# Performance work log

Hardware: AMD Instinct MI355X
Metric: run time of the kernel (lower is better)

Reference implementation:

```python
import jax, jax.numpy as jnp
import numpy as np

POOL_SIZE = 8
SEG_LEN = 100
N_CODEBOOKS = 4
VOCAB = 1024
EMB = 128
HID = 512
LAT = 256
NUM_CODES = 1024
BETA = 0.1
BATCH = 128


def _pool_matrix(T, P):
    # torch adaptive_avg_pool1d bin boundaries
    starts = np.floor(np.arange(P) * T / P).astype(int)
    ends = np.ceil((np.arange(P) + 1) * T / P).astype(int)
    M = np.zeros((T, P), np.float32)
    for i in range(P):
        M[starts[i]:ends[i], i] = 1.0 / (ends[i] - starts[i])
    return jnp.asarray(M)

_POOL = _pool_matrix(SEG_LEN, POOL_SIZE)


def _conv1d_same3(x, w, b):
    # x: (B, Cin, T), w: (Cout, Cin, 3), padding=1
    y = jax.lax.conv_general_dilated(x, w, (1,), [(1, 1)],
                                     dimension_numbers=('NCH', 'OIH', 'NCH'))
    return y + b[None, :, None]


def _encode(tokens, emb, c1w, c1b, c2w, c2b, c3w, c3b):
    # tokens: (B, T, C) int -> z_e (B, POOL_SIZE, LAT)
    B, T, C = tokens.shape
    x = emb[tokens]                      # (B, T, C, EMB)
    x = x.reshape(B, T, C * EMB).transpose(0, 2, 1)  # (B, C*EMB, T)
    x = jax.nn.relu(_conv1d_same3(x, c1w, c1b))
    x = jax.nn.relu(_conv1d_same3(x, c2w, c2b))
    x = jnp.einsum('bct,tp->bcp', x, _POOL)          # adaptive avg pool -> (B, HID, 8)
    x = jnp.einsum('bcp,oc->bpo', x, c3w[:, :, 0]) + c3b  # 1x1 conv -> (B, 8, LAT)
    return x


def _vq(z_e, codebook):
    # z_e: (B, L, D); eval-mode EMA quantizer (no buffer update)
    cb_sq = jnp.sum(codebook ** 2, axis=-1)          # (K,)
    dist = (jnp.sum(z_e ** 2, axis=-1, keepdims=True)
            - 2.0 * jnp.einsum('bld,kd->blk', z_e, codebook) + cb_sq)
    codes = jnp.argmin(dist, axis=-1)                # (B, L)
    z_q = codebook[codes]                            # gather (B, L, D)
    z_q_st = z_e + jax.lax.stop_gradient(z_q - z_e)
    commit = jnp.mean((z_e - jax.lax.stop_gradient(z_q)) ** 2)
    return z_q_st, codes, BETA * commit


def _decode(z_prev, z_curr, z_next, fc1w, fc1b, fc2w, fc2b, d1w, d1b, d2w, d2b):
    B = z_curr.shape[0]
    z = jnp.concatenate([z_prev, z_curr, z_next], axis=1).reshape(B, -1)  # (B, 3*8*LAT)
    h = jax.nn.relu(z @ fc1w.T + fc1b)
    h = jax.nn.relu(h @ fc2w.T + fc2b)               # (B, HID)
    h = jnp.broadcast_to(h[:, :, None], (B, HID, SEG_LEN))
    # ConvTranspose1d(k=3, pad=1, stride=1) == conv with flipped, transposed kernel
    w1 = jnp.flip(jnp.swapaxes(d1w, 0, 1), -1)       # (O, I, 3)
    h = jax.nn.relu(_conv1d_same3(h, w1, d1b))
    out = jnp.einsum('bct,cv->bvt', h, d2w[:, :, 0]) + d2b[None, :, None]  # (B, V*C, T)
    logits = out.reshape(B, N_CODEBOOKS, VOCAB, SEG_LEN).transpose(0, 3, 1, 2)
    return logits                                    # (B, T, C, V)


def _model(tokens_prev, tokens_curr, tokens_next, emb, conv1_w, conv1_b,
           conv2_w, conv2_b, conv3_w, conv3_b, codebook, fc1_w, fc1_b,
           fc2_w, fc2_b, deconv1_w, deconv1_b, deconv2_w, deconv2_b):
    enc = lambda t: _encode(t, emb, conv1_w, conv1_b, conv2_w, conv2_b, conv3_w, conv3_b)
    z_prev, _, vq_prev = _vq(enc(tokens_prev), codebook)
    z_curr, _, vq_curr = _vq(enc(tokens_curr), codebook)
    z_next, _, vq_next = _vq(enc(tokens_next), codebook)
    logits = _decode(z_prev, z_curr, z_next, fc1_w, fc1_b, fc2_w, fc2_b,
                     deconv1_w, deconv1_b, deconv2_w, deconv2_b)
    logp = jax.nn.log_softmax(logits, axis=-1)
    nll = -jnp.take_along_axis(logp, tokens_curr[..., None], axis=-1)[..., 0]
    recon_loss = jnp.mean(nll)
    vq_loss = vq_prev + vq_curr + vq_next
    centered = codebook - jnp.mean(codebook, axis=0, keepdims=True)
    diversity_loss = -jnp.mean(centered ** 2)
    total = recon_loss + vq_loss + 0.0 * diversity_loss  # variance_loss_scale=0.0
    return total


def setup_inputs() -> dict:
    key = jax.random.key(0)
    ks = jax.random.split(key, 20)
    s = 0.02
    n = lambda k, shape, sc=0.02: sc * jax.random.normal(k, shape, dtype=jnp.float32)
    return {
        'tokens_prev': jax.random.randint(ks[0], (BATCH, SEG_LEN, N_CODEBOOKS), 0, VOCAB),
        'tokens_curr': jax.random.randint(ks[1], (BATCH, SEG_LEN, N_CODEBOOKS), 0, VOCAB),
        'tokens_next': jax.random.randint(ks[2], (BATCH, SEG_LEN, N_CODEBOOKS), 0, VOCAB),
        'emb': n(ks[3], (VOCAB, EMB), 1.0),
        'conv1_w': n(ks[4], (HID, EMB * N_CODEBOOKS, 3)),
        'conv1_b': jnp.zeros((HID,), jnp.float32),
        'conv2_w': n(ks[5], (HID, HID, 3)),
        'conv2_b': jnp.zeros((HID,), jnp.float32),
        'conv3_w': n(ks[6], (LAT, HID, 1)),
        'conv3_b': jnp.zeros((LAT,), jnp.float32),
        'codebook': n(ks[7], (NUM_CODES, LAT), 1.0),
        'fc1_w': n(ks[8], (HID, LAT * POOL_SIZE * 3)),
        'fc1_b': jnp.zeros((HID,), jnp.float32),
        'fc2_w': n(ks[9], (HID, HID)),
        'fc2_b': jnp.zeros((HID,), jnp.float32),
        'deconv1_w': n(ks[10], (HID, HID, 3)),
        'deconv1_b': jnp.zeros((HID,), jnp.float32),
        'deconv2_w': n(ks[11], (HID, VOCAB * N_CODEBOOKS, 1)),
        'deconv2_b': jnp.zeros((VOCAB * N_CODEBOOKS,), jnp.float32),
    }


def reference(tokens_prev, tokens_curr, tokens_next, emb, conv1_w, conv1_b,
              conv2_w, conv2_b, conv3_w, conv3_b, codebook, fc1_w, fc1_b,
              fc2_w, fc2_b, deconv1_w, deconv1_b, deconv2_w, deconv2_b):
    return _model(tokens_prev, tokens_curr, tokens_next, emb, conv1_w, conv1_b,
                  conv2_w, conv2_b, conv3_w, conv3_b, codebook, fc1_w, fc1_b,
                  fc2_w, fc2_b, deconv1_w, deconv1_b, deconv2_w, deconv2_b)
```

## Files before the change

kernel.cpp:

```cpp
#include <hip/hip_runtime.h>
#include <math.h>

#define B_    128
#define T_    100
#define TPAD  104
#define CB_   4
#define EMB_  128
#define NROW  39936
#define ZOFF  131072

typedef __attribute__((ext_vector_type(8))) short short8;
typedef __attribute__((ext_vector_type(4))) short short4v;
typedef __attribute__((ext_vector_type(4))) float f32x4;

__device__ __forceinline__ short f2bf(float x) {
  unsigned u = __builtin_bit_cast(unsigned, x);
  u += 0x7fffu + ((u >> 16) & 1u);
  return (short)(u >> 16);
}
__device__ __forceinline__ float bf2f(short s) {
  unsigned u = ((unsigned)(unsigned short)s) << 16;
  return __builtin_bit_cast(float, u);
}

#define GLOAD_LDS(g, l) __builtin_amdgcn_global_load_lds( \
    (const __attribute__((address_space(1))) void*)(g),   \
    (__attribute__((address_space(3))) void*)(l), 16, 0, 0)

#define MFMA16(a, b, c) __builtin_amdgcn_mfma_f32_16x16x32_bf16(a, b, c, 0, 0, 0)
#define SWZ(row, slot) (((slot) + ((row) >> 1)) & 3)

__global__ void k_prep(const float* __restrict__ emb,
                       const float* __restrict__ c1w, const float* __restrict__ c2w,
                       const float* __restrict__ c3w, const float* __restrict__ cbk,
                       const float* __restrict__ fc1w, const float* __restrict__ fc2w,
                       const float* __restrict__ d1w, const float* __restrict__ d2w,
                       short* __restrict__ YbS, short* __restrict__ embB,
                       short* __restrict__ Wb1, short* __restrict__ Wb2,
                       short* __restrict__ c3wB, short* __restrict__ cbkB,
                       short* __restrict__ fc1wB, short* __restrict__ fc2wB,
                       short* __restrict__ SB, short* __restrict__ d2wTB,
                       float* __restrict__ cbsq) {
  __shared__ float tile[32][33];
  int bid = blockIdx.x;
  int id = bid * 256 + threadIdx.x;
  if (bid < 24581) {
    if (id < 1024) {
      int row = id >> 9, c = id & 511;
      long off = row ? ((long)(NROW + 1) * 512 + c) : c;
      YbS[off] = 0;
    } else if (id < 132096) {
      int l = id - 1024;
      embB[l] = f2bf(emb[l]);
    } else if (id < 132224) {
      embB[ZOFF + (id - 132096)] = 0;
    } else if (id < 1705088) {
      int local = id - 132224;
      const float* w = (local < 786432) ? c1w : c2w;
      short* o = (local < 786432) ? Wb1 : Wb2;
      int l2 = (local < 786432) ? local : local - 786432;
      int i = l2 & 511, oo = (l2 >> 9) & 511, tap = l2 >> 18;
      o[l2] = f2bf(w[oo * 1536 + i * 3 + tap]);
    } else if (id < 1836160) {
      int l = id - 1705088;
      c3wB[l] = f2bf(c3w[l]);
    } else if (id < 2098304) {
      int l = id - 1836160;
      cbkB[l] = f2bf(cbk[l]);
    } else if (id < 5244032) {
      int l = id - 2098304;
      fc1wB[l] = f2bf(fc1w[l]);
    } else if (id < 5506176) {
      int l = id - 5244032;
      fc2wB[l] = f2bf(fc2w[l]);
    } else if (id < 6292608) {
      int l = id - 5506176;
      int i = l & 511, o = (l >> 9) & 511, cls = l >> 18;
      const float* w = d1w + (i * 512 + o) * 3;
      float v;
      if (cls == 0)      v = w[0] + w[1];
      else if (cls == 1) v = w[0] + w[1] + w[2];
      else               v = w[1] + w[2];
      SB[(cls * 512 + o) * 512 + i] = f2bf(v);
    }
  } else if (bid < 26629) {
    int blk = bid - 24581;
    int bx = blk & 127, by = blk >> 7;
    int tx = threadIdx.x & 31, ty = threadIdx.x >> 5;
    #pragma unroll
    for (int j = 0; j < 32; j += 8)
      tile[ty + j][tx] = d2w[(by * 32 + ty + j) * 4096 + bx * 32 + tx];
    __syncthreads();
    #pragma unroll
    for (int j = 0; j < 32; j += 8)
      d2wTB[(bx * 32 + ty + j) * 512 + by * 32 + tx] = f2bf(tile[tx][ty + j]);
  } else {
    int idx = (bid - 26629) * 256 + threadIdx.x;
    int row = idx >> 6, lane = threadIdx.x & 63;
    float4 v = *(const float4*)&cbk[row * 256 + lane * 4];
    float s = v.x * v.x + v.y * v.y + v.z * v.z + v.w * v.w;
    #pragma unroll
    for (int m = 1; m < 64; m <<= 1) s += __shfl_xor(s, m);
    if (lane == 0) cbsq[row] = s;
  }
}

__global__ __launch_bounds__(256) void k_conv1_embed(const int* __restrict__ tok0,
                                                     const int* __restrict__ tok1,
                                                     const int* __restrict__ tok2,
                                                     const short* __restrict__ embB,
                                                     const short* __restrict__ Wb,
                                                     const float* __restrict__ bias,
                                                     short* __restrict__ Y) {
  __shared__ short sm[16896];
  int r0 = blockIdx.y * 128;
  int o0 = blockIdx.x * 128;
  int tid = threadIdx.x;
  int lane = tid & 63, wid = tid >> 6;
  int wm = wid >> 1, wn = wid & 1;
  int ls = lane >> 4, lr = lane & 15;
  int g = ((lane & 3) - ((lane >> 3) & 3)) & 3;

  int toff[3][4];
  #pragma unroll
  for (int i = 0; i < 3; ++i) {
    int q = wid + 4 * i;
    if (q < 9) {
      int rr = r0 - 1 + 16 * q + (lane >> 2);
      bool ok = (rr >= 0) && (rr < NROW);
      int sb = ok ? (rr / 104) : 0;
      int t = rr - sb * 104;
      ok = ok && (t < T_);
      int b = sb & 127, s = sb >> 7;
      const int* tokp = (s == 0) ? tok0 : (s == 1) ? tok1 : tok2;
      if (ok) {
        int4 tv = *(const int4*)&tokp[(b * T_ + t) * CB_];
        toff[i][0] = tv.x * EMB_; toff[i][1] = tv.y * EMB_;
        toff[i][2] = tv.z * EMB_; toff[i][3] = tv.w * EMB_;
      } else {
        toff[i][0] = toff[i][1] = toff[i][2] = toff[i][3] = ZOFF;
      }
    }
  }
  const short* gpw[9];
  short* lpw[9];
  #pragma unroll
  for (int i = 0; i < 9; ++i) {
    int q = wid + 4 * i;
    if (q >= 9 && q < 33) {
      int b = q - 9, tap = b >> 3, jj = b & 7;
      gpw[i] = Wb + (long)(tap * 512 + o0 + 16 * jj) * 512 + (long)(lane >> 2) * 512 + g * 8;
      lpw[i] = sm + q * 512;
    }
  }

  f32x4 acc[4][4] = {};
  #pragma unroll
  for (int cb = 0; cb < 4; ++cb) {
    #pragma unroll
    for (int kk = 0; kk < 4; ++kk) {
      __syncthreads();
      #pragma unroll
      for (int i = 0; i < 3; ++i) {
        int q = wid + 4 * i;
        if (q < 9) GLOAD_LDS(embB + toff[i][cb] + kk * 32 + g * 8, sm + q * 512);
      }
      #pragma unroll
      for (int i = 0; i < 9; ++i) {
        int q = wid + 4 * i;
        if (q >= 9 && q < 33) {
          GLOAD_LDS(gpw[i], lpw[i]);
          gpw[i] += 32;
        }
      }
      __syncthreads();
      const short8* A8 = (const short8*)sm;
      const short8* B8 = (const short8*)(sm + 4608);
      #pragma unroll
      for (int tap = 0; tap < 3; ++tap) {
        short8 a[4], b[4];
        #pragma unroll
        for (int m = 0; m < 4; ++m) {
          int row = wm * 64 + m * 16 + lr + tap;
          a[m] = A8[row * 4 + SWZ(row, ls)];
        }
        #pragma unroll
        for (int n = 0; n < 4; ++n) {
          int row = wn * 64 + n * 16 + lr;
          b[n] = B8[(tap * 128 + row) * 4 + SWZ(row, ls)];
        }
        #pragma unroll
        for (int m = 0; m < 4; ++m)
          #pragma unroll
          for (int n = 0; n < 4; ++n)
            acc[m][n] = MFMA16(a[m], b[n], acc[m][n]);
      }
    }
  }
  #pragma unroll
  for (int m = 0; m < 4; ++m) {
    #pragma unroll
    for (int n = 0; n < 4; ++n) {
      int col = o0 + wn * 64 + n * 16 + lr;
      float bv = bias[col];
      #pragma unroll
      for (int j = 0; j < 4; ++j) {
        int r = r0 + wm * 64 + m * 16 + ls * 4 + j;
        int t = r % TPAD;
        float v = (t < T_) ? fmaxf(acc[m][n][j] + bv, 0.f) : 0.f;
        Y[(long)r * 512 + col] = f2bf(v);
      }
    }
  }
}

__global__ __launch_bounds__(256) void k_conv3_mfma(const short* __restrict__ X,
                                                    const short* __restrict__ Wb,
                                                    const float* __restrict__ bias,
                                                    short* __restrict__ Y) {
  __shared__ short sm[16896];
  int r0 = blockIdx.y * 128;
  int o0 = blockIdx.x * 128;
  int tid = threadIdx.x;
  int lane = tid & 63, wid = tid >> 6;
  int wm = wid >> 1, wn = wid & 1;
  int ls = lane >> 4, lr = lane & 15;
  int g = ((lane & 3) - ((lane >> 3) & 3)) & 3;
  long laneoff = (long)(lane >> 2) * 512 + g * 8;

  const short* gp[9];
  const short* lp[9];
  #pragma unroll
  for (int i = 0; i < 9; ++i) {
    int q = wid + 4 * i;
    if (q < 33) {
      long base;
      const short* src;
      if (q < 9) { src = X; base = (long)(r0 - 1 + 16 * q) * 512; }
      else {
        int b = q - 9, tap = b >> 3, j = b & 7;
        src = Wb; base = (long)(tap * 512 + o0 + 16 * j) * 512;
      }
      gp[i] = src + base + laneoff;
      lp[i] = sm + q * 512;
    }
  }

  f32x4 acc[4][4] = {};
  for (int kc = 0; kc < 512; kc += 32) {
    __syncthreads();
    #pragma unroll
    for (int i = 0; i < 9; ++i) {
      int q = wid + 4 * i;
      if (q < 33) {
        GLOAD_LDS(gp[i], lp[i]);
        gp[i] += 32;
      }
    }
    __syncthreads();
    const short8* A8 = (const short8*)sm;
    const short8* B8 = (const short8*)(sm + 4608);
    #pragma unroll
    for (int tap = 0; tap < 3; ++tap) {
      short8 a[4], b[4];
      #pragma unroll
      for (int m = 0; m < 4; ++m) {
        int row = wm * 64 + m * 16 + lr + tap;
        a[m] = A8[row * 4 + SWZ(row, ls)];
      }
      #pragma unroll
      for (int n = 0; n < 4; ++n) {
        int row = wn * 64 + n * 16 + lr;
        b[n] = B8[(tap * 128 + row) * 4 + SWZ(row, ls)];
      }
      #pragma unroll
      for (int m = 0; m < 4; ++m)
        #pragma unroll
        for (int n = 0; n < 4; ++n)
          acc[m][n] = MFMA16(a[m], b[n], acc[m][n]);
    }
  }
  #pragma unroll
  for (int m = 0; m < 4; ++m) {
    #pragma unroll
    for (int n = 0; n < 4; ++n) {
      int col = o0 + wn * 64 + n * 16 + lr;
      float bv = bias[col];
      #pragma unroll
      for (int j = 0; j < 4; ++j) {
        int r = r0 + wm * 64 + m * 16 + ls * 4 + j;
        int t = r % TPAD;
        float v = (t < T_) ? fmaxf(acc[m][n][j] + bv, 0.f) : 0.f;
        Y[(long)r * 512 + col] = f2bf(v);
      }
    }
  }
}

__global__ __launch_bounds__(256) void k_gemm_mfma(const short* __restrict__ A,
                                                   const short* __restrict__ B,
                                                   float* __restrict__ C,
                                                   short* __restrict__ Cb,
                                                   const float* __restrict__ bias,
                                                   int K, int N, int relu) {
  __shared__ short sm[8192];
  int r0 = blockIdx.x * 128;
  int o0 = blockIdx.y * 128;
  int tid = threadIdx.x;
  int lane = tid & 63, wid = tid >> 6;
  int wm = wid >> 1, wn = wid & 1;
  int ls = lane >> 4, lr = lane & 15;
  int g = ((lane & 3) - ((lane >> 3) & 3)) & 3;
  long laneoff = (long)(lane >> 2) * K + g * 8;

  const short* gp[4];
  const short* lp[4];
  #pragma unroll
  for (int i = 0; i < 4; ++i) {
    int q = wid + 4 * i;
    const short* src;
    long base;
    if (q < 8) { src = A; base = (long)(r0 + 16 * q) * K; }
    else       { src = B; base = (long)(o0 + 16 * (q - 8)) * K; }
    gp[i] = src + base + laneoff;
    lp[i] = sm + q * 512;
  }

  f32x4 acc[4][4] = {};
  for (int kc = 0; kc < K; kc += 32) {
    __syncthreads();
    #pragma unroll
    for (int i = 0; i < 4; ++i) {
      GLOAD_LDS(gp[i], lp[i]);
      gp[i] += 32;
    }
    __syncthreads();
    const short8* A8 = (const short8*)sm;
    const short8* B8 = (const short8*)(sm + 4096);
    short8 a[4], b[4];
    #pragma unroll
    for (int m = 0; m < 4; ++m) {
      int row = wm * 64 + m * 16 + lr;
      a[m] = A8[row * 4 + SWZ(row, ls)];
    }
    #pragma unroll
    for (int n = 0; n < 4; ++n) {
      int row = wn * 64 + n * 16 + lr;
      b[n] = B8[row * 4 + SWZ(row, ls)];
    }
    #pragma unroll
    for (int m = 0; m < 4; ++m)
      #pragma unroll
      for (int n = 0; n < 4; ++n)
        acc[m][n] = MFMA16(a[m], b[n], acc[m][n]);
  }
  #pragma unroll
  for (int m = 0; m < 4; ++m) {
    #pragma unroll
    for (int n = 0; n < 4; ++n) {
      int col = o0 + wn * 64 + n * 16 + lr;
      float bv = bias ? bias[col] : 0.f;
      #pragma unroll
      for (int j = 0; j < 4; ++j) {
        int r = r0 + wm * 64 + m * 16 + ls * 4 + j;
        float v = acc[m][n][j] + bv;
        if (relu) v = fmaxf(v, 0.f);
        C[(long)r * N + col] = v;
        if (Cb) Cb[(long)r * N + col] = f2bf(v);
      }
    }
  }
}

__global__ __launch_bounds__(256) void k_dot_argmin(const short* __restrict__ A,
                                                    const short* __restrict__ B,
                                                    const float* __restrict__ cbsq,
                                                    float* __restrict__ apv,
                                                    int* __restrict__ api) {
  __shared__ short sm[8192];
  __shared__ float svv[128][2];
  __shared__ int sii[128][2];
  const int K = 256;
  int r0 = blockIdx.x * 128;
  int o0 = blockIdx.y * 128;
  int tid = threadIdx.x;
  int lane = tid & 63, wid = tid >> 6;
  int wm = wid >> 1, wn = wid & 1;
  int ls = lane >> 4, lr = lane & 15;
  int g = ((lane & 3) - ((lane >> 3) & 3)) & 3;
  long laneoff = (long)(lane >> 2) * K + g * 8;

  const short* gp[4];
  const short* lp[4];
  #pragma unroll
  for (int i = 0; i < 4; ++i) {
    int q = wid + 4 * i;
    const short* src;
    long base;
    if (q < 8) { src = A; base = (long)(r0 + 16 * q) * K; }
    else       { src = B; base = (long)(o0 + 16 * (q - 8)) * K; }
    gp[i] = src + base + laneoff;
    lp[i] = sm + q * 512;
  }

  f32x4 acc[4][4] = {};
  #pragma unroll
  for (int kc = 0; kc < K; kc += 32) {
    __syncthreads();
    #pragma unroll
    for (int i = 0; i < 4; ++i) {
      GLOAD_LDS(gp[i], lp[i]);
      gp[i] += 32;
    }
    __syncthreads();
    const short8* A8 = (const short8*)sm;
    const short8* B8 = (const short8*)(sm + 4096);
    short8 a[4], b[4];
    #pragma unroll
    for (int m = 0; m < 4; ++m) {
      int row = wm * 64 + m * 16 + lr;
      a[m] = A8[row * 4 + SWZ(row, ls)];
    }
    #pragma unroll
    for (int n = 0; n < 4; ++n) {
      int row = wn * 64 + n * 16 + lr;
      b[n] = B8[row * 4 + SWZ(row, ls)];
    }
    #pragma unroll
    for (int m = 0; m < 4; ++m)
      #pragma unroll
      for (int n = 0; n < 4; ++n)
        acc[m][n] = MFMA16(a[m], b[n], acc[m][n]);
  }
  float cq[4];
  #pragma unroll
  for (int n = 0; n < 4; ++n) cq[n] = cbsq[o0 + wn * 64 + n * 16 + lr];
  #pragma unroll
  for (int m = 0; m < 4; ++m) {
    #pragma unroll
    for (int j = 0; j < 4; ++j) {
      float bv = 3.4e38f; int bi = 0x7fffffff;
      #pragma unroll
      for (int n = 0; n < 4; ++n) {
        int col = o0 + wn * 64 + n * 16 + lr;
        float v = cq[n] - 2.f * acc[m][n][j];
        if (v < bv || (v == bv && col < bi)) { bv = v; bi = col; }
      }
      #pragma unroll
      for (int d = 1; d < 16; d <<= 1) {
        float ov = __shfl_xor(bv, d);
        int oi = __shfl_xor(bi, d);
        if (ov < bv || (ov == bv && oi < bi)) { bv = ov; bi = oi; }
      }
      if (lr == 0) {
        int rl = wm * 64 + m * 16 + ls * 4 + j;
        svv[rl][wn] = bv;
        sii[rl][wn] = bi;
      }
    }
  }
  __syncthreads();
  if (tid < 128) {
    float v0 = svv[tid][0], v1 = svv[tid][1];
    int i0 = sii[tid][0], i1 = sii[tid][1];
    bool t1 = (v1 < v0) || (v1 == v0 && i1 < i0);
    apv[(long)(r0 + tid) * 8 + blockIdx.y] = t1 ? v1 : v0;
    api[(long)(r0 + tid) * 8 + blockIdx.y] = t1 ? i1 : i0;
  }
}

__global__ __launch_bounds__(256) void k_vq_combine(const float* __restrict__ apv,
                                                    const int* __restrict__ api,
                                                    const float* __restrict__ ze,
                                                    const float* __restrict__ cb,
                                                    const short* __restrict__ cbkB,
                                                    short* __restrict__ zallB,
                                                    float* __restrict__ commit_part) {
  __shared__ float sv[256];
  __shared__ int ksb;
  int row = blockIdx.x, tid = threadIdx.x;
  if (tid == 0) {
    float bv = apv[(long)row * 8]; int bi = api[(long)row * 8];
    #pragma unroll
    for (int j = 1; j < 8; ++j) {
      float v = apv[(long)row * 8 + j]; int i = api[(long)row * 8 + j];
      if (v < bv || (v == bv && i < bi)) { bv = v; bi = i; }
    }
    ksb = bi;
  }
  __syncthreads();
  int ks = ksb;
  float zq = cb[ks * 256 + tid];
  float zev = ze[(long)row * 256 + tid];
  int s = row >> 10, bp = row & 1023;
  int b = bp >> 3, p = bp & 7;
  zallB[b * 6144 + s * 2048 + p * 256 + tid] = cbkB[ks * 256 + tid];
  float d = zev - zq;
  sv[tid] = d * d;
  __syncthreads();
  for (int off = 128; off; off >>= 1) { if (tid < off) sv[tid] += sv[tid + off]; __syncthreads(); }
  if (tid == 0) commit_part[row] = sv[0];
}

__global__ __launch_bounds__(256) void k_gemm_mfma_sk(const short* __restrict__ A,
                                                      const short* __restrict__ B,
                                                      float* __restrict__ part,
                                                      int M, int N, int K,
                                                      int kchunk, int KS, long bgstride) {
  __shared__ short sm[8192];
  int r0 = blockIdx.x * 128;
  int o0 = blockIdx.y * 128;
  int bz = blockIdx.z;
  int g = bz / KS, zz = bz - g * KS;
  const short* Bg = B + (long)g * bgstride;
  int k0 = zz * kchunk;
  int tid = threadIdx.x;
  int lane = tid & 63, wid = tid >> 6;
  int wm = wid >> 1, wn = wid & 1;
  int ls = lane >> 4, lr = lane & 15;
  int gsl = ((lane & 3) - ((lane >> 3) & 3)) & 3;
  long laneoff = (long)(lane >> 2) * K + gsl * 8 + k0;

  const short* gp[4];
  const short* lp[4];
  #pragma unroll
  for (int i = 0; i < 4; ++i) {
    int q = wid + 4 * i;
    const short* src;
    long base;
    if (q < 8) { src = A;  base = (long)(r0 + 16 * q) * K; }
    else       { src = Bg; base = (long)(o0 + 16 * (q - 8)) * K; }
    gp[i] = src + base + laneoff;
    lp[i] = sm + q * 512;
  }

  f32x4 acc[4][4] = {};
  for (int kc = 0; kc < kchunk; kc += 32) {
    __syncthreads();
    #pragma unroll
    for (int i = 0; i < 4; ++i) {
      GLOAD_LDS(gp[i], lp[i]);
      gp[i] += 32;
    }
    __syncthreads();
    const short8* A8 = (const short8*)sm;
    const short8* B8 = (const short8*)(sm + 4096);
    short8 a[4], b[4];
    #pragma unroll
    for (int m = 0; m < 4; ++m) {
      int row = wm * 64 + m * 16 + lr;
      a[m] = A8[row * 4 + SWZ(row, ls)];
    }
    #pragma unroll
    for (int n = 0; n < 4; ++n) {
      int row = wn * 64 + n * 16 + lr;
      b[n] = B8[row * 4 + SWZ(row, ls)];
    }
    #pragma unroll
    for (int m = 0; m < 4; ++m)
      #pragma unroll
      for (int n = 0; n < 4; ++n)
        acc[m][n] = MFMA16(a[m], b[n], acc[m][n]);
  }
  float* P = part + (long)bz * M * N;
  #pragma unroll
  for (int m = 0; m < 4; ++m) {
    #pragma unroll
    for (int n = 0; n < 4; ++n) {
      int col = o0 + wn * 64 + n * 16 + lr;
      #pragma unroll
      for (int j = 0; j < 4; ++j) {
        int r = r0 + wm * 64 + m * 16 + ls * 4 + j;
        P[(long)r * N + col] = acc[m][n][j];
      }
    }
  }
}

__global__ void k_reduce_bf16(const float* __restrict__ part, short* __restrict__ Cb,
                              const float* __restrict__ bias, int N, int MN,
                              int KS, int relu, int total4) {
  int id = blockIdx.x * 256 + threadIdx.x;
  if (id >= total4) return;
  int e = id * 4;
  int g = e / MN;
  int rem = e - g * MN;
  const float* base = part + (long)g * KS * MN + rem;
  float4 s = *(const float4*)base;
  for (int j = 1; j < KS; ++j) {
    float4 v = *(const float4*)(base + (long)j * MN);
    s.x += v.x; s.y += v.y; s.z += v.z; s.w += v.w;
  }
  int c = rem % N;
  s.x += bias[c]; s.y += bias[c + 1]; s.z += bias[c + 2]; s.w += bias[c + 3];
  if (relu) {
    s.x = fmaxf(s.x, 0.f); s.y = fmaxf(s.y, 0.f);
    s.z = fmaxf(s.z, 0.f); s.w = fmaxf(s.w, 0.f);
  }
  short4v o;
  o[0] = f2bf(s.x); o[1] = f2bf(s.y); o[2] = f2bf(s.z); o[3] = f2bf(s.w);
  *(short4v*)&Cb[(long)g * MN + rem] = o;
}

__global__ void k_pool(const short* __restrict__ Xg, short* __restrict__ pooledB) {
  int id = blockIdx.x * 256 + threadIdx.x;
  int row = id >> 6, cg = id & 63;
  int s = row >> 10, bp = row & 1023;
  int b = bp >> 3, p = bp & 7;
  int t0 = (p * 25) >> 1;
  const short8* src = (const short8*)(Xg + (long)((s * 128 + b) * TPAD + t0) * 512) + cg;
  float acc[8] = {};
  #pragma unroll
  for (int j = 0; j < 13; ++j) {
    short8 v = src[j * 64];
    #pragma unroll
    for (int k = 0; k < 8; ++k) acc[k] += bf2f(v[k]);
  }
  short8 o;
  #pragma unroll
  for (int k = 0; k < 8; ++k) o[k] = f2bf(acc[k] * (1.f / 13.f));
  ((short8*)pooledB)[(long)row * 64 + cg] = o;
}

__global__ __launch_bounds__(256) void k_logits_lse_recon(const float* __restrict__ part,
                                                          const float* __restrict__ d2b,
                                                          const int* __restrict__ tok,
                                                          float* __restrict__ rpart2) {
  __shared__ float row[1024];
  __shared__ float sm[256];
  int blk = blockIdx.x;
  int cb_i = blk & 3, b = (blk >> 2) & 127, cls = blk >> 9;
  int m = cls * 128 + b;
  const float* p0 = part + (long)m * 4096 + cb_i * 1024;
  const float* p1 = p0 + (long)384 * 4096;
  const float* bb = d2b + cb_i * 1024;
  int tid = threadIdx.x;
  float v[4];
  #pragma unroll
  for (int j = 0; j < 4; ++j) {
    int c = tid + 256 * j;
    v[j] = p0[c] + p1[c] + bb[c];
    row[c] = v[j];
  }
  float mx = fmaxf(fmaxf(v[0], v[1]), fmaxf(v[2], v[3]));
  sm[tid] = mx; __syncthreads();
  for (int off = 128; off; off >>= 1) { if (tid < off) sm[tid] = fmaxf(sm[tid], sm[tid + off]); __syncthreads(); }
  float gm = sm[0]; __syncthreads();
  float e = expf(v[0] - gm) + expf(v[1] - gm) + expf(v[2] - gm) + expf(v[3] - gm);
  sm[tid] = e; __syncthreads();
  for (int off = 128; off; off >>= 1) { if (tid < off) sm[tid] += sm[tid + off]; __syncthreads(); }
  float lse = gm + logf(sm[0]);
  __syncthreads();
  float val = 0.f;
  if (cls == 1) {
    if (tid < 98) {
      int tk = tok[(b * T_ + tid + 1) * CB_ + cb_i];
      val = lse - row[tk];
    }
  } else if (tid == 0) {
    int t = (cls == 0) ? 0 : 99;
    int tk = tok[(b * T_ + t) * CB_ + cb_i];
    val = lse - row[tk];
  }
  sm[tid] = val; __syncthreads();
  for (int off = 128; off; off >>= 1) { if (tid < off) sm[tid] += sm[tid + off]; __syncthreads(); }
  if (tid == 0) rpart2[blk] = sm[0];
}

__global__ void k_final(const float* __restrict__ rpart2, const float* __restrict__ cpart,
                        float* __restrict__ out) {
  __shared__ float sm[256];
  __shared__ float rs;
  int tid = threadIdx.x;
  float r = 0.f;
  #pragma unroll
  for (int j = 0; j < 6; ++j) r += rpart2[tid + 256 * j];
  sm[tid] = r; __syncthreads();
  for (int off = 128; off; off >>= 1) { if (tid < off) sm[tid] += sm[tid + off]; __syncthreads(); }
  if (tid == 0) rs = sm[0];
  __syncthreads();
  float c = 0.f;
  #pragma unroll
  for (int j = 0; j < 12; ++j) c += cpart[tid + 256 * j];
  sm[tid] = c; __syncthreads();
  for (int off = 128; off; off >>= 1) { if (tid < off) sm[tid] += sm[tid + off]; __syncthreads(); }
  if (tid == 0) out[0] = rs / 51200.f + 0.1f * (sm[0] / 262144.f);
}

extern "C" void kernel_launch(void* const* d_in, const int* in_sizes, int n_in,
                              void* d_out, int out_size, void* d_ws, size_t ws_size,
                              hipStream_t stream) {
  const int*   tok_prev = (const int*)d_in[0];
  const int*   tok_curr = (const int*)d_in[1];
  const int*   tok_next = (const int*)d_in[2];
  const float* emb  = (const float*)d_in[3];
  const float* c1w  = (const float*)d_in[4];
  const float* c1b  = (const float*)d_in[5];
  const float* c2w  = (const float*)d_in[6];
  const float* c2b  = (const float*)d_in[7];
  const float* c3w  = (const float*)d_in[8];
  const float* c3b  = (const float*)d_in[9];
  const float* cbk  = (const float*)d_in[10];
  const float* fc1w = (const float*)d_in[11];
  const float* fc1b = (const float*)d_in[12];
  const float* fc2w = (const float*)d_in[13];
  const float* fc2b = (const float*)d_in[14];
  const float* d1w  = (const float*)d_in[15];
  const float* d1b  = (const float*)d_in[16];
  const float* d2w  = (const float*)d_in[17];
  const float* d2b  = (const float*)d_in[18];

  float* ws = (float*)d_ws;
  short* XbS = (short*)ws;
  short* YbS = (short*)(ws + 10224128);
  float* fp  = ws + 2 * 10224128;
  short* Wb1    = (short*)fp;
  short* Wb2    = (short*)(fp + 393216);
  short* c3wB   = (short*)(fp + 786432);
  short* cbkB   = (short*)(fp + 851968);
  short* pooledB= (short*)(fp + 983040);
  float* ze     = fp + 1769472;
  short* zeB    = (short*)(fp + 2555904);
  short* fc1wB  = (short*)(fp + 2949120);
  short* fc2wB  = (short*)(fp + 4521984);
  short* SB     = (short*)(fp + 4653056);
  short* d2wTB  = (short*)(fp + 5046272);
  float* part   = fp + 6094848;
  float* cbsq   = part + 3145728;
  short* zallB  = (short*)(cbsq + 1024);
  float* cpart  = cbsq + 1024 + 393216;
  short* h1B    = (short*)(cpart + 3072);
  short* h2B    = (short*)(cpart + 35840);
  short* h2cB   = (short*)(cpart + 68608);
  float* rpart2 = cpart + 166912;
  float* apv    = cpart + 168448;
  int*   api    = (int*)(cpart + 193024);
  short* embB   = (short*)(cpart + 217600);

  const short* Yv = YbS + 512;
  short* Xc = XbS + 512;

  k_prep<<<26885, 256, 0, stream>>>(emb, c1w, c2w, c3w, cbk, fc1w, fc2w, d1w, d2w,
                                    YbS, embB, Wb1, Wb2, c3wB, cbkB, fc1wB, fc2wB,
                                    SB, d2wTB, cbsq);

  k_conv1_embed<<<dim3(4, 312), 256, 0, stream>>>(tok_prev, tok_curr, tok_next,
                                                  embB, Wb1, c1b, (short*)Yv);
  k_conv3_mfma <<<dim3(4, 312), 256, 0, stream>>>(Yv, Wb2, c2b, Xc);
  k_pool       <<<768, 256, 0, stream>>>(Xc, pooledB);
  k_gemm_mfma  <<<dim3(24, 2), 256, 0, stream>>>(pooledB, c3wB, ze, zeB, c3b, 512, 256, 0);
  k_dot_argmin <<<dim3(24, 8), 256, 0, stream>>>(zeB, cbkB, cbsq, apv, api);
  k_vq_combine <<<3072, 256, 0, stream>>>(apv, api, ze, cbk, cbkB, zallB, cpart);

  k_gemm_mfma_sk<<<dim3(1, 4, 16), 256, 0, stream>>>(zallB, fc1wB, part, 128, 512, 6144, 384, 16, 0);
  k_reduce_bf16 <<<64, 256, 0, stream>>>(part, h1B, fc1b, 512, 65536, 16, 1, 16384);
  k_gemm_mfma_sk<<<dim3(1, 4, 8), 256, 0, stream>>>(h1B, fc2wB, part, 128, 512, 512, 64, 8, 0);
  k_reduce_bf16 <<<64, 256, 0, stream>>>(part, h2B, fc2b, 512, 65536, 8, 1, 16384);
  k_gemm_mfma_sk<<<dim3(1, 4, 24), 256, 0, stream>>>(h2B, SB, part, 128, 512, 512, 64, 8, 262144);
  k_reduce_bf16 <<<192, 256, 0, stream>>>(part, h2cB, d1b, 512, 65536, 8, 1, 49152);
  k_gemm_mfma_sk<<<dim3(3, 32, 2), 256, 0, stream>>>(h2cB, d2wTB, part, 384, 4096, 512, 256, 2, 0);
  k_logits_lse_recon<<<1536, 256, 0, stream>>>(part, d2b, tok_curr, rpart2);

  k_final<<<1, 256, 0, stream>>>(rpart2, cpart, (float*)d_out);
}
```

Before: 274.5 us.

## Double-buffer LDS tiles in conv MFMA kernels to overlap loads with compute

Both conv GEMM kernels now keep two LDS buffers. Each step issues the global-to-LDS loads for the next K-chunk before running the MFMAs on the current one, then waits on vmcnt and a single barrier. This hides global load latency behind matrix math and removes one barrier per iteration. LDS use per block doubles to about 67 KB, which can reduce how many blocks fit on each CU.

Measured after the change: 260.3 us, median of 2. 5.2% less time.

```diff
diff --git a/kernel.cpp b/kernel.cpp
--- a/kernel.cpp
+++ b/kernel.cpp
@@ -29,6 +29,12 @@
 
 #define MFMA16(a, b, c) __builtin_amdgcn_mfma_f32_16x16x32_bf16(a, b, c, 0, 0, 0)
 #define SWZ(row, slot) (((slot) + ((row) >> 1)) & 3)
+
+#define STEP_SYNC() do {                                   \
+    asm volatile("s_waitcnt vmcnt(0)" ::: "memory");       \
+    __builtin_amdgcn_s_barrier();                          \
+    __builtin_amdgcn_sched_barrier(0);                     \
+  } while (0)
 
 __global__ void k_prep(const float* __restrict__ emb,
                        const float* __restrict__ c1w, const float* __restrict__ c2w,
@@ -112,7 +118,7 @@
                                                      const short* __restrict__ Wb,
                                                      const float* __restrict__ bias,
                                                      short* __restrict__ Y) {
-  __shared__ short sm[16896];
+  __shared__ short sm[2][16896];
   int r0 = blockIdx.y * 128;
   int o0 = blockIdx.x * 128;
   int tid = threadIdx.x;
@@ -143,59 +149,66 @@
     }
   }
   const short* gpw[9];
-  short* lpw[9];
   #pragma unroll
   for (int i = 0; i < 9; ++i) {
     int q = wid + 4 * i;
     if (q >= 9 && q < 33) {
       int b = q - 9, tap = b >> 3, jj = b & 7;
       gpw[i] = Wb + (long)(tap * 512 + o0 + 16 * jj) * 512 + (long)(lane >> 2) * 512 + g * 8;
-      lpw[i] = sm + q * 512;
-    }
-  }
+    }
+  }
+
+  #pragma unroll
+  for (int i = 0; i < 3; ++i) {
+    int q = wid + 4 * i;
+    if (q < 9) GLOAD_LDS(embB + toff[i][0] + g * 8, &sm[0][q * 512]);
+  }
+  #pragma unroll
+  for (int i = 0; i < 9; ++i) {
+    int q = wid + 4 * i;
+    if (q >= 9 && q < 33) { GLOAD_LDS(gpw[i], &sm[0][q * 512]); gpw[i] += 32; }
+  }
+  STEP_SYNC();
 
   f32x4 acc[4][4] = {};
   #pragma unroll
-  for (int cb = 0; cb < 4; ++cb) {
-    #pragma unroll
-    for (int kk = 0; kk < 4; ++kk) {
-      __syncthreads();
+  for (int u = 0; u < 16; ++u) {
+    const int cur = u & 1;
+    if (u < 15) {
+      const int cb2 = (u + 1) >> 2, kk2 = (u + 1) & 3;
       #pragma unroll
       for (int i = 0; i < 3; ++i) {
         int q = wid + 4 * i;
-        if (q < 9) GLOAD_LDS(embB + toff[i][cb] + kk * 32 + g * 8, sm + q * 512);
+        if (q < 9) GLOAD_LDS(embB + toff[i][cb2] + kk2 * 32 + g * 8, &sm[cur ^ 1][q * 512]);
       }
       #pragma unroll
       for (int i = 0; i < 9; ++i) {
         int q = wid + 4 * i;
-        if (q >= 9 && q < 33) {
-          GLOAD_LDS(gpw[i], lpw[i]);
-          gpw[i] += 32;
-        }
-      }
-      __syncthreads();
-      const short8* A8 = (const short8*)sm;
-      const short8* B8 = (const short8*)(sm + 4608);
-      #pragma unroll
-      for (int tap = 0; tap < 3; ++tap) {
-        short8 a[4], b[4];
+        if (q >= 9 && q < 33) { GLOAD_LDS(gpw[i], &sm[cur ^ 1][q * 512]); gpw[i] += 32; }
+      }
+    }
+    const short8* A8 = (const short8*)sm[cur];
+    const short8* B8 = (const short8*)(sm[cur] + 4608);
+    #pragma unroll
+    for (int tap = 0; tap < 3; ++tap) {
+      short8 a[4], b[4];
+      #pragma unroll
+      for (int m = 0; m < 4; ++m) {
+        int row = wm * 64 + m * 16 + lr + tap;
+        a[m] = A8[row * 4 + SWZ(row, ls)];
+      }
+      #pragma unroll
+      for (int n = 0; n < 4; ++n) {
+        int row = wn * 64 + n * 16 + lr;
+        b[n] = B8[(tap * 128 + row) * 4 + SWZ(row, ls)];
+      }
+      #pragma unroll
+      for (int m = 0; m < 4; ++m)
         #pragma unroll
-        for (int m = 0; m < 4; ++m) {
-          int row = wm * 64 + m * 16 + lr + tap;
-          a[m] = A8[row * 4 + SWZ(row, ls)];
-        }
-        #pragma unroll
-        for (int n = 0; n < 4; ++n) {
-          int row = wn * 64 + n * 16 + lr;
-          b[n] = B8[(tap * 128 + row) * 4 + SWZ(row, ls)];
-        }
-        #pragma unroll
-        for (int m = 0; m < 4; ++m)
-          #pragma unroll
-          for (int n = 0; n < 4; ++n)
-            acc[m][n] = MFMA16(a[m], b[n], acc[m][n]);
-      }
-    }
+        for (int n = 0; n < 4; ++n)
+          acc[m][n] = MFMA16(a[m], b[n], acc[m][n]);
+    }
+    STEP_SYNC();
   }
   #pragma unroll
   for (int m = 0; m < 4; ++m) {
@@ -218,7 +231,7 @@
                                                     const short* __restrict__ Wb,
                                                     const float* __restrict__ bias,
                                                     short* __restrict__ Y) {
-  __shared__ short sm[16896];
+  __shared__ short sm[2][16896];
   int r0 = blockIdx.y * 128;
   int o0 = blockIdx.x * 128;
   int tid = threadIdx.x;
@@ -229,7 +242,6 @@
   long laneoff = (long)(lane >> 2) * 512 + g * 8;
 
   const short* gp[9];
-  const short* lp[9];
   #pragma unroll
   for (int i = 0; i < 9; ++i) {
     int q = wid + 4 * i;
@@ -242,24 +254,29 @@
         src = Wb; base = (long)(tap * 512 + o0 + 16 * j) * 512;
       }
       gp[i] = src + base + laneoff;
-      lp[i] = sm + q * 512;
-    }
-  }
+    }
+  }
+
+  #pragma unroll
+  for (int i = 0; i < 9; ++i) {
+    int q = wid + 4 * i;
+    if (q < 33) { GLOAD_LDS(gp[i], &sm[0][q * 512]); gp[i] += 32; }
+  }
+  STEP_SYNC();
 
   f32x4 acc[4][4] = {};
-  for (int kc = 0; kc < 512; kc += 32) {
-    __syncthreads();
-    #pragma unroll
-    for (int i = 0; i < 9; ++i) {
-      int q = wid + 4 * i;
-      if (q < 33) {
-        GLOAD_LDS(gp[i], lp[i]);
-        gp[i] += 32;
-      }
-    }
-    __syncthreads();
-    const short8* A8 = (const short8*)sm;
-    const short8* B8 = (const short8*)(sm + 4608);
+  #pragma unroll
+  for (int u = 0; u < 16; ++u) {
+    const int cur = u & 1;
+    if (u < 15) {
+      #pragma unroll
+      for (int i = 0; i < 9; ++i) {
+        int q = wid + 4 * i;
+        if (q < 33) { GLOAD_LDS(gp[i], &sm[cur ^ 1][q * 512]); gp[i] += 32; }
+      }
+    }
+    const short8* A8 = (const short8*)sm[cur];
+    const short8* B8 = (const short8*)(sm[cur] + 4608);
     #pragma unroll
     for (int tap = 0; tap < 3; ++tap) {
       short8 a[4], b[4];
@@ -279,6 +296,7 @@
         for (int n = 0; n < 4; ++n)
           acc[m][n] = MFMA16(a[m], b[n], acc[m][n]);
     }
+    STEP_SYNC();
   }
   #pragma unroll
   for (int m = 0; m < 4; ++m) {
```
